# Kernel optimization log

Hardware: AMD Instinct MI355X
Metric: run time of the kernel (lower is better)

## Reference

```python
import jax, jax.numpy as jnp
import numpy as np
from jax import lax

THRESHOLD = 10.0  # p-norm threshold in HSEM
BN_EPS = 1e-5
DN = ('NCHW', 'OIHW', 'NCHW')


def setup_inputs() -> dict:
    key = jax.random.key(0)
    ks = jax.random.split(key, 9)
    b, c, h, w = 2, 256, 64, 64
    c_out = 512
    # scale x so pairwise L2 distances straddle the threshold (dense-ish hypergraph)
    x = jax.random.normal(ks[0], (b, c, h, w), dtype=jnp.float32) * 0.4
    fc_w = jax.random.normal(ks[1], (c, c), dtype=jnp.float32) * 0.02
    fc_b = jax.random.normal(ks[2], (c,), dtype=jnp.float32) * 0.02
    bn_gamma = jnp.ones((c,), dtype=jnp.float32)
    bn_beta = jnp.zeros((c,), dtype=jnp.float32)
    down_w = jax.random.normal(ks[3], (c, c, 3, 3), dtype=jnp.float32) * 0.02
    down_b = jax.random.normal(ks[4], (c,), dtype=jnp.float32) * 0.02
    out_w = jax.random.normal(ks[5], (c_out, c, 1, 1), dtype=jnp.float32) * 0.02
    out_b = jax.random.normal(ks[6], (c_out,), dtype=jnp.float32) * 0.02
    return {"x": x, "fc_w": fc_w, "fc_b": fc_b, "bn_gamma": bn_gamma,
            "bn_beta": bn_beta, "down_w": down_w, "down_b": down_b,
            "out_w": out_w, "out_b": out_b}


def _mean_agg(path, X):
    # path: [b, n_tgt, n_src], X: [b, n_src, d]; mean aggregation with inf->0 masking
    s = jnp.sum(path, axis=2, keepdims=True)           # [b, n_tgt, 1]
    norm = jnp.where(s > 0, 1.0 / jnp.where(s > 0, s, 1.0), 0.0)
    return norm * jnp.matmul(path, X)


def reference(x, fc_w, fc_b, bn_gamma, bn_beta, down_w, down_b, out_w, out_b):
    b, c, h, w = x.shape
    n = h * w
    xf = x.reshape(b, c, n).transpose(0, 2, 1)          # [b, n, c]
    # cdist (euclidean): ||a-b|| via expansion
    sq = jnp.sum(xf * xf, axis=-1)                      # [b, n]
    d2 = sq[:, :, None] + sq[:, None, :] - 2.0 * jnp.einsum('bnc,bmc->bnm', xf, xf)
    dist = jnp.sqrt(jnp.maximum(d2, 0.0))               # [b, n, n]
    hg = (dist < THRESHOLD).astype(x.dtype)             # dynamic hypergraph incidence
    # HyPConv: fc -> v2e (H^T) -> e2v (H)
    y = jnp.einsum('bnc,dc->bnd', xf, fc_w) + fc_b      # Linear(c1, c2)
    E = _mean_agg(jnp.swapaxes(hg, 1, 2), y)            # vertex -> edge
    v = _mean_agg(hg, E)                                # edge -> vertex
    xf = v + xf                                         # residual
    x4 = xf.transpose(0, 2, 1).reshape(b, c, h, w)
    # BatchNorm2d (training-mode batch statistics, biased var)
    mean = jnp.mean(x4, axis=(0, 2, 3))
    var = jnp.var(x4, axis=(0, 2, 3))
    xn = (x4 - mean[None, :, None, None]) * lax.rsqrt(var + BN_EPS)[None, :, None, None]
    xn = xn * bn_gamma[None, :, None, None] + bn_beta[None, :, None, None]
    xa = xn * jax.nn.sigmoid(xn)                        # SiLU
    # Downsample: pad (right=1, bottom=1) then 3x3 stride-2 VALID conv
    xp = jnp.pad(xa, ((0, 0), (0, 0), (0, 1), (0, 1)))
    xd = lax.conv_general_dilated(xp, down_w, (2, 2), 'VALID', dimension_numbers=DN)
    xd = xd + down_b[None, :, None, None]
    out = lax.conv_general_dilated(xd, out_w, (1, 1), 'VALID', dimension_numbers=DN)
    out = out + out_b[None, :, None, None]
    return out
```

## Files before the change

### kernel.cpp

```cpp
#include <hip/hip_runtime.h>
#include <hip/hip_bf16.h>
#include <math.h>

#define NPIX 4096
#define CH   256

#define OFF_XP    0u
#define OFF_XR    1048576u
#define OFF_VB    2097152u
#define OFF_TBS   3145728u
#define OFF_TBS2  4194304u
#define OFF_HG    5242880u
#define OFF_SQ    6291456u
#define OFF_PART  6299648u
#define OFF_BNSS  6365184u
#define OFF_DINV  6365696u
#define OFF_W3P   6373888u
#define OFF_WFCP  6668800u
#define OFF_WOUTP 6701568u

typedef __attribute__((ext_vector_type(8))) short bf16x8;
typedef __attribute__((ext_vector_type(16))) float f32x16;

static __device__ __forceinline__ short f2b(float f) {
  __hip_bfloat16 h = __float2bfloat16(f);
  return *reinterpret_cast<short*>(&h);
}
static __device__ __forceinline__ float b2f(short s) {
  union { unsigned u; float f; } r;
  r.u = ((unsigned)(unsigned short)s) << 16;
  return r.f;
}

static __device__ __forceinline__ bf16x8 byte2bf(unsigned byte) {
  union { unsigned u[4]; bf16x8 h; } r;
  r.u[0] = ((byte * 0x8001u) & 0x10001u) * 0x3F80u;
  r.u[1] = (((byte >> 2) * 0x8001u) & 0x10001u) * 0x3F80u;
  r.u[2] = (((byte >> 4) * 0x8001u) & 0x10001u) * 0x3F80u;
  r.u[3] = (((byte >> 6) * 0x8001u) & 0x10001u) * 0x3F80u;
  return r.h;
}

static __device__ __forceinline__ size_t packoff(int m, int c) {
  return ((size_t)((m >> 5) * 16 + (c >> 4)) * 2 + ((c >> 3) & 1)) * 256 + (m & 31) * 8 + (c & 7);
}

__global__ __launch_bounds__(256) void k_front2(const float* __restrict__ x,
                                                short* __restrict__ xp,
                                                float* __restrict__ sq,
                                                const float* __restrict__ fc_w,
                                                const float* __restrict__ ow,
                                                const float* __restrict__ dw,
                                                short* __restrict__ wfcp,
                                                short* __restrict__ woutp,
                                                short* __restrict__ w3p) {
  __shared__ float lds[256][33];
  __shared__ float red2[8][32];
  const int bid = blockIdx.x;
  const int t = threadIdx.x;
  if (bid < 256) {
    const int b = bid >> 7;
    const int n0 = (bid & 127) * 32;
    const float* xb = x + (size_t)b * CH * NPIX + n0;
    const int j = t & 31, cg8 = t >> 5;
#pragma unroll 4
    for (int it = 0; it < 32; ++it) {
      const int c = it * 8 + cg8;
      lds[c][j] = xb[(size_t)c * NPIX + j];
    }
    __syncthreads();
    {
      const int n = t & 31, cg = t >> 5;
      float s = 0.f;
#pragma unroll 8
      for (int i = 0; i < 32; ++i) {
        const float v = lds[cg * 32 + i][n];
        s += v * v;
      }
      red2[cg][n] = s;
    }
    short* xpb = xp + (size_t)b * NPIX * CH;
#pragma unroll
    for (int i = 0; i < 4; ++i) {
      const int f = i * 256 + t;
      const int n = f & 31, c0 = (f >> 5) * 8;
      short tmp[8];
#pragma unroll
      for (int k = 0; k < 8; ++k) tmp[k] = f2b(lds[c0 + k][n]);
      short* dst = xpb + packoff(n0 + n, c0);
      *(short4*)dst = *(short4*)&tmp[0];
      *(short4*)(dst + 4) = *(short4*)&tmp[4];
    }
    __syncthreads();
    if (t < 32) {
      float s = 0.f;
#pragma unroll
      for (int cg = 0; cg < 8; ++cg) s += red2[cg][t];
      sq[b * NPIX + n0 + t] = s;
    }
  } else {
    const int i = (bid - 256) * 256 + t;
    if (i < 65536) {
      wfcp[packoff(i >> 8, i & 255)] = f2b(fc_w[i]);
    } else if (i < 196608) {
      const int j = i - 65536;
      woutp[packoff(j >> 8, j & 255)] = f2b(ow[j]);
    } else {
      const int j = i - 196608;
      const int oc = j / 2304;
      const int rem = j % 2304;
      const int c = rem / 9, tap = rem % 9;
      const size_t off = ((size_t)((tap * 8 + (oc >> 5)) * 16 + (c >> 4)) * 2 + ((c >> 3) & 1)) * 256
                       + (oc & 31) * 8 + (c & 7);
      w3p[off] = f2b(dw[j]);
    }
  }
}

__global__ __launch_bounds__(128, 2) void k_gram4(const short* __restrict__ xp,
                                                  const float* __restrict__ sq,
                                                  unsigned* __restrict__ hgbit) {
  const int b = blockIdx.z;
  int tt = blockIdx.x;
  int bi = (int)((65.0f - sqrtf(4225.0f - 8.0f * (float)tt)) * 0.5f);
  bi = bi < 0 ? 0 : (bi > 31 ? 31 : bi);
  while (bi * (65 - bi) / 2 > tt) --bi;
  while ((bi + 1) * (64 - bi) / 2 <= tt) ++bi;
  const int bj = bi + (tt - bi * (65 - bi) / 2);
  const int i0 = bi * 128, j0 = bj * 128;

  const int t = threadIdx.x;
  const int lane = t & 63, w = t >> 6;
  const int c = lane & 31, h = lane >> 5;
  const short* xb = xp + (size_t)b * NPIX * CH;
  const int ibase = i0 + w * 64;
  const int jbase = j0;

  f32x16 acc[2][4];
#pragma unroll
  for (int m = 0; m < 2; ++m)
#pragma unroll
    for (int n = 0; n < 4; ++n)
#pragma unroll
      for (int r = 0; r < 16; ++r) acc[m][n][r] = 0.f;

  const short* pa = xb + (size_t)(ibase >> 5) * 8192 + lane * 8;
  const short* pb = xb + (size_t)(jbase >> 5) * 8192 + lane * 8;

#pragma unroll 2
  for (int kb = 0; kb < 16; ++kb) {
    const bf16x8 a0 = *(const bf16x8*)(pa + kb * 512);
    const bf16x8 a1 = *(const bf16x8*)(pa + 8192 + kb * 512);
    bf16x8 bb[4];
#pragma unroll
    for (int n = 0; n < 4; ++n) bb[n] = *(const bf16x8*)(pb + (size_t)n * 8192 + kb * 512);
#pragma unroll
    for (int n = 0; n < 4; ++n) {
      acc[0][n] = __builtin_amdgcn_mfma_f32_32x32x16_bf16(a0, bb[n], acc[0][n], 0, 0, 0);
      acc[1][n] = __builtin_amdgcn_mfma_f32_32x32x16_bf16(a1, bb[n], acc[1][n], 0, 0, 0);
    }
  }

  const int sqb = b * NPIX;
#pragma unroll
  for (int m = 0; m < 2; ++m) {
    float4 sqa[4];
#pragma unroll
    for (int q = 0; q < 4; ++q)
      sqa[q] = *(const float4*)(sq + sqb + ibase + m * 32 + q * 8 + 4 * h);
#pragma unroll
    for (int n = 0; n < 4; ++n) {
      const float sj = sq[sqb + jbase + n * 32 + c];
      const int wj = (jbase + n * 32) >> 5;
      unsigned mmask = 0u;
#pragma unroll
      for (int q = 0; q < 4; ++q) {
        const float sqq[4] = {sqa[q].x, sqa[q].y, sqa[q].z, sqa[q].w};
#pragma unroll
        for (int rr = 0; rr < 4; ++rr) {
          const int reg = q * 4 + rr;
          const float d2 = sqq[rr] + sj - 2.f * acc[m][n][reg];
          const bool cond = d2 < 100.f;
          const unsigned long long bal = __ballot(cond);
          if ((lane & 31) == reg) {
            const int row = ibase + m * 32 + rr + 8 * q + 4 * h;
            const unsigned wd = h ? (unsigned)(bal >> 32) : (unsigned)bal;
            hgbit[(size_t)(sqb + row) * 128 + wj] = wd;
          }
          mmask |= (cond ? 1u : 0u) << (rr + 8 * q + 4 * h);
        }
      }
      const unsigned merged = mmask | (unsigned)__shfl_xor((int)mmask, 32, 64);
      if (h == 0) {
        const int colg = jbase + n * 32 + c;
        hgbit[(size_t)(sqb + colg) * 128 + ((ibase + m * 32) >> 5)] = merged;
      }
    }
  }
}

__global__ __launch_bounds__(256) void k_fcdinv(const short* __restrict__ wfcp,
                                                const short* __restrict__ xp,
                                                short* __restrict__ C,
                                                const float* __restrict__ bias,
                                                const unsigned* __restrict__ hg,
                                                float* __restrict__ dinvf) {
  const int bid = blockIdx.x;
  const int t = threadIdx.x;
  if (bid >= 256) {
    const int row = (bid - 256) * 4 + (t >> 6);
    const int l = t & 63;
    const unsigned w0 = hg[(size_t)row * 128 + l * 2];
    const unsigned w1 = hg[(size_t)row * 128 + l * 2 + 1];
    int n = __popc(w0) + __popc(w1);
#pragma unroll
    for (int off = 32; off; off >>= 1) n += __shfl_down(n, off);
    if (l == 0) dinvf[row] = 1.0f / (float)n;
    return;
  }
  const int b = bid >> 7;
  const short* xpb = xp + (size_t)b * NPIX * CH;
  short* Cb = C + ((size_t)b << 20);
  const int l = t & 63, wid = t >> 6;
  const int m0 = ((bid >> 6) & 1) * 128 + wid * 32, n0 = (bid & 63) * 64;
  const int col = l & 31, half = l >> 5;
  f32x16 acc[2];
#pragma unroll
  for (int nt = 0; nt < 2; ++nt)
#pragma unroll
    for (int r = 0; r < 16; ++r) acc[nt][r] = 0.f;
  const short* pa = wfcp + (size_t)(m0 >> 5) * 8192 + l * 8;
  const short* pb = xpb + (size_t)(n0 >> 5) * 8192 + l * 8;
#pragma unroll 4
  for (int kb = 0; kb < 16; ++kb) {
    const bf16x8 a = *(const bf16x8*)(pa + kb * 512);
    const bf16x8 b0 = *(const bf16x8*)(pb + kb * 512);
    const bf16x8 b1 = *(const bf16x8*)(pb + 8192 + kb * 512);
    acc[0] = __builtin_amdgcn_mfma_f32_32x32x16_bf16(a, b0, acc[0], 0, 0, 0);
    acc[1] = __builtin_amdgcn_mfma_f32_32x32x16_bf16(a, b1, acc[1], 0, 0, 0);
  }
  const int cb = m0 >> 5;
#pragma unroll
  for (int nt = 0; nt < 2; ++nt) {
    const int node = n0 + nt * 32 + col;
    short* dst = Cb + ((size_t)cb * 512 + (node >> 3)) * 256 + (node & 7);
#pragma unroll
    for (int q = 0; q < 4; ++q)
#pragma unroll
      for (int rr = 0; rr < 4; ++rr) {
        const int c31 = rr + 8 * q + 4 * half;
        dst[c31 * 8] = f2b(acc[nt][q * 4 + rr] + bias[m0 + c31]);
      }
  }
}

__global__ __launch_bounds__(256) void k_hgemm_t4(const short* __restrict__ tbs,
                                                  const unsigned* __restrict__ hg,
                                                  const float* __restrict__ dinvf,
                                                  short* __restrict__ tbs2) {
  __shared__ float red[4][64][33];
  const int b = blockIdx.z;
  const int n0 = blockIdx.x * 64;
  const int cbp = blockIdx.y;
  const int ks = threadIdx.x >> 6;
  const int l = threadIdx.x & 63;
  const int col = l & 31, half = l >> 5;
  const int sh8 = half * 8;

  f32x16 acc00, acc01, acc10, acc11;
#pragma unroll
  for (int r = 0; r < 16; ++r) { acc00[r] = 0.f; acc01[r] = 0.f; acc10[r] = 0.f; acc11[r] = 0.f; }

  const short* pa0 = tbs + ((size_t)b << 20) + ((size_t)(cbp * 2) * 512 + half) * 256
                   + col * 8 + ks * 32768;
  const short* pa1 = pa0 + 131072;
  const uint4* hrow0 = (const uint4*)((const unsigned char*)hg
                     + ((size_t)b * NPIX + n0 + col) * 512 + ks * 128);
  const uint4* hrow1 = (const uint4*)((const unsigned char*)hg
                     + ((size_t)b * NPIX + n0 + 32 + col) * 512 + ks * 128);

#pragma unroll 2
  for (int o = 0; o < 8; ++o) {
    const uint4 wq0 = hrow0[o];
    const uint4 wq1 = hrow1[o];
    const unsigned ww0[4] = {wq0.x, wq0.y, wq0.z, wq0.w};
    const unsigned ww1[4] = {wq1.x, wq1.y, wq1.z, wq1.w};
#pragma unroll
    for (int s = 0; s < 4; ++s) {
      const bf16x8 a00 = *(const bf16x8*)(pa0);
      const bf16x8 a01 = *(const bf16x8*)(pa0 + 512);
      const bf16x8 a10 = *(const bf16x8*)(pa1);
      const bf16x8 a11 = *(const bf16x8*)(pa1 + 512);
      pa0 += 1024; pa1 += 1024;
      const bf16x8 b0 = byte2bf((ww0[s] >> sh8) & 0xFFu);
      const bf16x8 b1 = byte2bf((ww0[s] >> (16 + sh8)) & 0xFFu);
      const bf16x8 c0 = byte2bf((ww1[s] >> sh8) & 0xFFu);
      const bf16x8 c1 = byte2bf((ww1[s] >> (16 + sh8)) & 0xFFu);
      acc00 = __builtin_amdgcn_mfma_f32_32x32x16_bf16(a00, b0, acc00, 0, 0, 0);
      acc00 = __builtin_amdgcn_mfma_f32_32x32x16_bf16(a01, b1, acc00, 0, 0, 0);
      acc10 = __builtin_amdgcn_mfma_f32_32x32x16_bf16(a10, b0, acc10, 0, 0, 0);
      acc10 = __builtin_amdgcn_mfma_f32_32x32x16_bf16(a11, b1, acc10, 0, 0, 0);
      acc01 = __builtin_amdgcn_mfma_f32_32x32x16_bf16(a00, c0, acc01, 0, 0, 0);
      acc01 = __builtin_amdgcn_mfma_f32_32x32x16_bf16(a01, c1, acc01, 0, 0, 0);
      acc11 = __builtin_amdgcn_mfma_f32_32x32x16_bf16(a10, c0, acc11, 0, 0, 0);
      acc11 = __builtin_amdgcn_mfma_f32_32x32x16_bf16(a11, c1, acc11, 0, 0, 0);
    }
  }

#pragma unroll
  for (int r = 0; r < 16; ++r) { red[ks][l][r] = acc00[r]; red[ks][l][16 + r] = acc10[r]; }
  __syncthreads();
  {
    const int n = n0 + col;
    const float dinv = dinvf[b * NPIX + n];
    short* dst0 = tbs2 + ((size_t)b << 20) + ((size_t)(cbp * 2) * 512 + (n >> 3)) * 256 + (n & 7);
    short* dst1 = dst0 + 131072;
#pragma unroll
    for (int rj = 0; rj < 8; ++rj) {
      const int reg = ks * 8 + rj;
      const float s = red[0][l][reg] + red[1][l][reg] + red[2][l][reg] + red[3][l][reg];
      const int rm = reg & 15;
      const int c31 = (rm & 3) + 8 * (rm >> 2) + 4 * half;
      (reg < 16 ? dst0 : dst1)[c31 * 8] = f2b(s * dinv);
    }
  }
  __syncthreads();
#pragma unroll
  for (int r = 0; r < 16; ++r) { red[ks][l][r] = acc01[r]; red[ks][l][16 + r] = acc11[r]; }
  __syncthreads();
  {
    const int n = n0 + 32 + col;
    const float dinv = dinvf[b * NPIX + n];
    short* dst0 = tbs2 + ((size_t)b << 20) + ((size_t)(cbp * 2) * 512 + (n >> 3)) * 256 + (n & 7);
    short* dst1 = dst0 + 131072;
#pragma unroll
    for (int rj = 0; rj < 8; ++rj) {
      const int reg = ks * 8 + rj;
      const float s = red[0][l][reg] + red[1][l][reg] + red[2][l][reg] + red[3][l][reg];
      const int rm = reg & 15;
      const int c31 = (rm & 3) + 8 * (rm >> 2) + 4 * half;
      (reg < 16 ? dst0 : dst1)[c31 * 8] = f2b(s * dinv);
    }
  }
}

__global__ __launch_bounds__(256) void k_hgemm_n4(const unsigned* __restrict__ hg,
                                                  const short* __restrict__ tbs2,
                                                  const float* __restrict__ dinvf,
                                                  const short* __restrict__ xp,
                                                  short* __restrict__ vb,
                                                  float* __restrict__ part) {
  __shared__ float red[4][64][33];
  __shared__ float bnp[128];
  const int b = blockIdx.z;
  const int cbp = blockIdx.x;
  const int m0 = blockIdx.y * 64;
  const int ks = threadIdx.x >> 6;
  const int l = threadIdx.x & 63;
  const int col = l & 31, half = l >> 5;
  const int sh8 = half * 8;
  if (threadIdx.x < 128) bnp[threadIdx.x] = 0.f;

  f32x16 acc00, acc01, acc10, acc11;
#pragma unroll
  for (int r = 0; r < 16; ++r) { acc00[r] = 0.f; acc01[r] = 0.f; acc10[r] = 0.f; acc11[r] = 0.f; }

  const short* pb0 = tbs2 + ((size_t)b << 20) + ((size_t)(cbp * 2) * 512 + half) * 256
                   + col * 8 + ks * 32768;
  const short* pb1 = pb0 + 131072;
  const uint4* hrow0 = (const uint4*)((const unsigned char*)hg
                     + ((size_t)b * NPIX + m0 + col) * 512 + ks * 128);
  const uint4* hrow1 = (const uint4*)((const unsigned char*)hg
                     + ((size_t)b * NPIX + m0 + 32 + col) * 512 + ks * 128);

#pragma unroll 2
  for (int o = 0; o < 8; ++o) {
    const uint4 wq0 = hrow0[o];
    const uint4 wq1 = hrow1[o];
    const unsigned ww0[4] = {wq0.x, wq0.y, wq0.z, wq0.w};
    const unsigned ww1[4] = {wq1.x, wq1.y, wq1.z, wq1.w};
#pragma unroll
    for (int s = 0; s < 4; ++s) {
      const bf16x8 b00 = *(const bf16x8*)(pb0);
      const bf16x8 b01 = *(const bf16x8*)(pb0 + 512);
      const bf16x8 b10 = *(const bf16x8*)(pb1);
      const bf16x8 b11 = *(const bf16x8*)(pb1 + 512);
      pb0 += 1024; pb1 += 1024;
      const bf16x8 a0 = byte2bf((ww0[s] >> sh8) & 0xFFu);
      const bf16x8 a1 = byte2bf((ww0[s] >> (16 + sh8)) & 0xFFu);
      const bf16x8 a2 = byte2bf((ww1[s] >> sh8) & 0xFFu);
      const bf16x8 a3 = byte2bf((ww1[s] >> (16 + sh8)) & 0xFFu);
      acc00 = __builtin_amdgcn_mfma_f32_32x32x16_bf16(a0, b00, acc00, 0, 0, 0);
      acc00 = __builtin_amdgcn_mfma_f32_32x32x16_bf16(a1, b01, acc00, 0, 0, 0);
      acc01 = __builtin_amdgcn_mfma_f32_32x32x16_bf16(a0, b10, acc01, 0, 0, 0);
      acc01 = __builtin_amdgcn_mfma_f32_32x32x16_bf16(a1, b11, acc01, 0, 0, 0);
      acc10 = __builtin_amdgcn_mfma_f32_32x32x16_bf16(a2, b00, acc10, 0, 0, 0);
      acc10 = __builtin_amdgcn_mfma_f32_32x32x16_bf16(a3, b01, acc10, 0, 0, 0);
      acc11 = __builtin_amdgcn_mfma_f32_32x32x16_bf16(a2, b10, acc11, 0, 0, 0);
      acc11 = __builtin_amdgcn_mfma_f32_32x32x16_bf16(a3, b11, acc11, 0, 0, 0);
    }
  }

  const short* xpb = xp + (size_t)b * NPIX * CH;
#pragma unroll
  for (int r = 0; r < 16; ++r) { red[ks][l][r] = acc00[r]; red[ks][l][16 + r] = acc01[r]; }
  __syncthreads();
  {
    const int cc = cbp * 64 + col;
#pragma unroll
    for (int rj = 0; rj < 8; ++rj) {
      const int reg = ks * 8 + rj;
      const float s = red[0][l][reg] + red[1][l][reg] + red[2][l][reg] + red[3][l][reg];
      const int rm = reg & 15;
      const int r = m0 + (rm & 3) + 8 * (rm >> 2) + 4 * half;
      const int ccc = cc + (reg < 16 ? 0 : 32);
      const size_t o = ((size_t)(b * NPIX + r)) * CH + ccc;
      const short sv = f2b(s * dinvf[b * NPIX + r] + b2f(xpb[packoff(r, ccc)]));
      vb[o] = sv;
      const float vr = b2f(sv);
      const int ci = col + (reg < 16 ? 0 : 32);
      atomicAdd(&bnp[ci], vr);
      atomicAdd(&bnp[64 + ci], vr * vr);
    }
  }
  __syncthreads();
#pragma unroll
  for (int r = 0; r < 16; ++r) { red[ks][l][r] = acc10[r]; red[ks][l][16 + r] = acc11[r]; }
  __syncthreads();
  {
    const int cc = cbp * 64 + col;
#pragma unroll
    for (int rj = 0; rj < 8; ++rj) {
      const int reg = ks * 8 + rj;
      const float s = red[0][l][reg] + red[1][l][reg] + red[2][l][reg] + red[3][l][reg];
      const int rm = reg & 15;
      const int r = m0 + 32 + (rm & 3) + 8 * (rm >> 2) + 4 * half;
      const int ccc = cc + (reg < 16 ? 0 : 32);
      const size_t o = ((size_t)(b * NPIX + r)) * CH + ccc;
      const short sv = f2b(s * dinvf[b * NPIX + r] + b2f(xpb[packoff(r, ccc)]));
      vb[o] = sv;
      const float vr = b2f(sv);
      const int ci = col + (reg < 16 ? 0 : 32);
      atomicAdd(&bnp[ci], vr);
      atomicAdd(&bnp[64 + ci], vr * vr);
    }
  }
  __syncthreads();
  if (threadIdx.x < 128) {
    const int slot = b * 64 + blockIdx.y;
    part[((size_t)(cbp * 128 + slot)) * 128 + threadIdx.x] = bnp[threadIdx.x];
  }
}

__global__ void k_bnfin(const float* __restrict__ part, const float* __restrict__ gamma,
                        const float* __restrict__ beta, float* __restrict__ bnss) {
  const int t = threadIdx.x;
  const int cbp = t >> 6, ch = t & 63;
  float s = 0.f, ss = 0.f;
  for (int i = 0; i < 128; ++i) {
    const float* p = part + ((size_t)(cbp * 128 + i)) * 128;
    s += p[ch];
    ss += p[64 + ch];
  }
  const float mean = s * (1.f / 8192.f);
  const float var = ss * (1.f / 8192.f) - mean * mean;
  const float inv = rsqrtf(var + 1e-5f);
  const float sc = gamma[t] * inv;
  bnss[t] = sc;
  bnss[256 + t] = beta[t] - mean * sc;
}

__global__ void k_bnapply3(const short* __restrict__ vb, const float* __restrict__ bnss,
                           short* __restrict__ xpp) {
  const int i = blockIdx.x * 256 + threadIdx.x;
  const short4 sv = reinterpret_cast<const short4*>(vb)[i];
  const int c0 = (i & 63) * 4;
  const int n = (i >> 6) & 4095;
  const int b = i >> 18;
  const float4 sc = *(const float4*)(bnss + c0);
  const float4 sh = *(const float4*)(bnss + 256 + c0);
  const float u0 = b2f(sv.x) * sc.x + sh.x;
  const float u1 = b2f(sv.y) * sc.y + sh.y;
  const float u2 = b2f(sv.z) * sc.z + sh.z;
  const float u3 = b2f(sv.w) * sc.w + sh.w;
  short4 o;
  o.x = f2b(u0 / (1.f + expf(-u0)));
  o.y = f2b(u1 / (1.f + expf(-u1)));
  o.z = f2b(u2 / (1.f + expf(-u2)));
  o.w = f2b(u3 / (1.f + expf(-u3)));
  const int ih = n >> 6, iw = n & 63;
  const int p = iw & 1, ow = iw >> 1;
  const size_t off = ((size_t)(((b * 2 + p) * 64 + ih) * 16 + (c0 >> 4)) * 2 + ((c0 >> 3) & 1)) * 256
                   + ow * 8 + (c0 & 7);
  *(short4*)(xpp + off) = o;
}

__global__ __launch_bounds__(64) void k_conv5(const short* __restrict__ xpp,
                                              const short* __restrict__ w3p,
                                              float* __restrict__ convp) {
  const int ocg = blockIdx.x;
  const int oh = blockIdx.y;
  const int bz = blockIdx.z;
  const int b = bz & 1, cs = bz >> 1;
  const int l = threadIdx.x;
  const int col = l & 31;
  const bf16x8 zv = {0, 0, 0, 0, 0, 0, 0, 0};

  f32x16 acc;
#pragma unroll
  for (int r = 0; r < 16; ++r) acc[r] = 0.f;

  for (int kh = 0; kh < 3; ++kh) {
    const int ih = 2 * oh + kh;
    if (ih >= 64) continue;
#pragma unroll
    for (int kw = 0; kw < 3; ++kw) {
      const int p = kw & 1;
      const short* pa = xpp + ((size_t)((b * 2 + p) * 64 + ih) * 16 + cs * 4) * 512
                      + l * 8 + (kw == 2 ? 8 : 0);
      const short* pb = w3p + ((size_t)((kh * 3 + kw) * 8 + ocg) * 16 + cs * 4) * 512 + l * 8;
      const bool kill = (kw == 2) && (col == 31);
#pragma unroll
      for (int kb = 0; kb < 4; ++kb) {
        bf16x8 a = *(const bf16x8*)(pa + kb * 512);
        if (kill) a = zv;
        const bf16x8 bb = *(const bf16x8*)(pb + kb * 512);
        acc = __builtin_amdgcn_mfma_f32_32x32x16_bf16(a, bb, acc, 0, 0, 0);
      }
    }
  }
  const int half = l >> 5;
  const int oc = ocg * 32 + col;
#pragma unroll
  for (int q = 0; q < 4; ++q)
#pragma unroll
    for (int rr = 0; rr < 4; ++rr) {
      const int ow = rr + 8 * q + 4 * half;
      convp[((size_t)bz * 1024 + oh * 32 + ow) * 256 + oc] = acc[q * 4 + rr];
    }
}

__global__ void k_convmerge3(const float* __restrict__ convp, const float* __restrict__ db,
                             short* __restrict__ xdtb) {
  const int i = blockIdx.x * 256 + threadIdx.x;
  const int b = i >> 16, px = (i >> 6) & 1023, oc0 = (i & 63) * 4;
  const size_t base = ((size_t)px) * 256 + oc0;
  const float4 h0 = *(const float4*)(convp + ((size_t)(0 + b) << 18) + base);
  const float4 h1 = *(const float4*)(convp + ((size_t)(2 + b) << 18) + base);
  const float4 h2 = *(const float4*)(convp + ((size_t)(4 + b) << 18) + base);
  const float4 h3 = *(const float4*)(convp + ((size_t)(6 + b) << 18) + base);
  const float4 bv = *(const float4*)(db + oc0);
  short4 o;
  o.x = f2b(h0.x + h1.x + h2.x + h3.x + bv.x);
  o.y = f2b(h0.y + h1.y + h2.y + h3.y + bv.y);
  o.z = f2b(h0.z + h1.z + h2.z + h3.z + bv.z);
  o.w = f2b(h0.w + h1.w + h2.w + h3.w + bv.w);
  const size_t off = ((size_t)((b * 32 + (px >> 5)) * 16 + (oc0 >> 4)) * 2 + ((oc0 >> 3) & 1)) * 256
                   + (px & 31) * 8 + (oc0 & 7);
  *(short4*)(xdtb + off) = o;
}

__global__ __launch_bounds__(256) void k_mfma_nt2(const short* __restrict__ woutp,
                                                  const short* __restrict__ xdtb,
                                                  float* __restrict__ C,
                                                  const float* __restrict__ bias) {
  const int b = blockIdx.z;
  xdtb += (size_t)b * 1024 * CH;
  C += (size_t)b * 512 * 1024;
  const int t = threadIdx.x, l = t & 63, wid = t >> 6;
  const int m0 = blockIdx.y * 128 + wid * 32, n0 = blockIdx.x * 64;
  const int col = l & 31, half = l >> 5;
  f32x16 acc[2];
#pragma unroll
  for (int nt = 0; nt < 2; ++nt)
#pragma unroll
    for (int r = 0; r < 16; ++r) acc[nt][r] = 0.f;
  const short* pa = woutp + (size_t)(m0 >> 5) * 8192 + l * 8;
  const short* pb = xdtb + (size_t)(n0 >> 5) * 8192 + l * 8;
#pragma unroll 4
  for (int kb = 0; kb < 16; ++kb) {
    const bf16x8 a = *(const bf16x8*)(pa + kb * 512);
    const bf16x8 b0 = *(const bf16x8*)(pb + kb * 512);
    const bf16x8 b1 = *(const bf16x8*)(pb + 8192 + kb * 512);
    acc[0] = __builtin_amdgcn_mfma_f32_32x32x16_bf16(a, b0, acc[0], 0, 0, 0);
    acc[1] = __builtin_amdgcn_mfma_f32_32x32x16_bf16(a, b1, acc[1], 0, 0, 0);
  }
#pragma unroll
  for (int nt = 0; nt < 2; ++nt) {
#pragma unroll
    for (int q = 0; q < 4; ++q)
#pragma unroll
      for (int rr = 0; rr < 4; ++rr) {
        const int row = m0 + rr + 8 * q + 4 * half;
        const int cc = n0 + nt * 32 + col;
        C[(size_t)row * 1024 + cc] = acc[nt][q * 4 + rr] + bias[row];
      }
  }
}

extern "C" void kernel_launch(void* const* d_in, const int* in_sizes, int n_in,
                              void* d_out, int out_size, void* d_ws, size_t ws_size,
                              hipStream_t stream) {
  const float* x     = (const float*)d_in[0];
  const float* fc_w  = (const float*)d_in[1];
  const float* fc_b  = (const float*)d_in[2];
  const float* gamma = (const float*)d_in[3];
  const float* beta  = (const float*)d_in[4];
  const float* dw    = (const float*)d_in[5];
  const float* db    = (const float*)d_in[6];
  const float* ow    = (const float*)d_in[7];
  const float* ob    = (const float*)d_in[8];

  float* ws   = (float*)d_ws;
  short* xp   = (short*)(ws + OFF_XP);
  float* convp= ws + OFF_XP;
  short* vb   = (short*)(ws + OFF_VB);
  short* tbs  = (short*)(ws + OFF_TBS);
  short* xdtb = (short*)(ws + OFF_TBS);
  short* tbs2 = (short*)(ws + OFF_TBS2);
  short* xpp  = (short*)(ws + OFF_TBS2);
  unsigned* hg = (unsigned*)(ws + OFF_HG);
  float* sqv  = ws + OFF_SQ;
  float* part = ws + OFF_PART;
  float* bnss = ws + OFF_BNSS;
  float* dinvf= ws + OFF_DINV;
  short* w3p  = (short*)(ws + OFF_W3P);
  short* wfcp = (short*)(ws + OFF_WFCP);
  short* woutp= (short*)(ws + OFF_WOUTP);
  float* out  = (float*)d_out;

  k_front2<<<3328, 256, 0, stream>>>(x, xp, sqv, fc_w, ow, dw, wfcp, woutp, w3p);
  k_gram4<<<dim3(528, 1, 2), 128, 0, stream>>>(xp, sqv, hg);
  k_fcdinv<<<2304, 256, 0, stream>>>(wfcp, xp, tbs, fc_b, hg, dinvf);
  k_hgemm_t4<<<dim3(64, 4, 2), 256, 0, stream>>>(tbs, hg, dinvf, tbs2);
  k_hgemm_n4<<<dim3(4, 64, 2), 256, 0, stream>>>(hg, tbs2, dinvf, xp, vb, part);
  k_bnfin<<<1, 256, 0, stream>>>(part, gamma, beta, bnss);
  k_bnapply3<<<2048, 256, 0, stream>>>(vb, bnss, xpp);
  k_conv5<<<dim3(8, 32, 8), 64, 0, stream>>>(xpp, w3p, convp);
  k_convmerge3<<<512, 256, 0, stream>>>(convp, db, xdtb);
  k_mfma_nt2<<<dim3(16, 4, 2), 256, 0, stream>>>(woutp, xdtb, out, ob);
}
```

Baseline: 140.4 us.

## Double split-K waves in hypergraph GEMMs and move BN statistics to separate kernel

Both hypergraph aggregation GEMMs now use 512 threads per block, splitting the K dimension across 8 waves instead of 4, with a larger shared-memory reduction buffer. The aim is more waves per block to hide the latency of the global loads. The per-element shared atomics that accumulated BatchNorm sums in the second GEMM are removed, and a new k_bnstat kernel recomputes per-channel sums from vb instead. This adds a kernel launch and a re-read of vb, and the larger shared buffer may lower occupancy.

```diff
diff --git a/kernel.cpp b/kernel.cpp
--- a/kernel.cpp
+++ b/kernel.cpp
@@ -254,11 +254,11 @@
   }
 }
 
-__global__ __launch_bounds__(256) void k_hgemm_t4(const short* __restrict__ tbs,
+__global__ __launch_bounds__(512) void k_hgemm_t5(const short* __restrict__ tbs,
                                                   const unsigned* __restrict__ hg,
                                                   const float* __restrict__ dinvf,
                                                   short* __restrict__ tbs2) {
-  __shared__ float red[4][64][33];
+  __shared__ float red[8][64][33];
   const int b = blockIdx.z;
   const int n0 = blockIdx.x * 64;
   const int cbp = blockIdx.y;
@@ -272,15 +272,15 @@
   for (int r = 0; r < 16; ++r) { acc00[r] = 0.f; acc01[r] = 0.f; acc10[r] = 0.f; acc11[r] = 0.f; }
 
   const short* pa0 = tbs + ((size_t)b << 20) + ((size_t)(cbp * 2) * 512 + half) * 256
-                   + col * 8 + ks * 32768;
+                   + col * 8 + ks * 16384;
   const short* pa1 = pa0 + 131072;
   const uint4* hrow0 = (const uint4*)((const unsigned char*)hg
-                     + ((size_t)b * NPIX + n0 + col) * 512 + ks * 128);
+                     + ((size_t)b * NPIX + n0 + col) * 512 + ks * 64);
   const uint4* hrow1 = (const uint4*)((const unsigned char*)hg
-                     + ((size_t)b * NPIX + n0 + 32 + col) * 512 + ks * 128);
-
-#pragma unroll 2
-  for (int o = 0; o < 8; ++o) {
+                     + ((size_t)b * NPIX + n0 + 32 + col) * 512 + ks * 64);
+
+#pragma unroll
+  for (int o = 0; o < 4; ++o) {
     const uint4 wq0 = hrow0[o];
     const uint4 wq1 = hrow1[o];
     const unsigned ww0[4] = {wq0.x, wq0.y, wq0.z, wq0.w};
@@ -316,9 +316,11 @@
     short* dst0 = tbs2 + ((size_t)b << 20) + ((size_t)(cbp * 2) * 512 + (n >> 3)) * 256 + (n & 7);
     short* dst1 = dst0 + 131072;
 #pragma unroll
-    for (int rj = 0; rj < 8; ++rj) {
-      const int reg = ks * 8 + rj;
-      const float s = red[0][l][reg] + red[1][l][reg] + red[2][l][reg] + red[3][l][reg];
+    for (int rj = 0; rj < 4; ++rj) {
+      const int reg = ks * 4 + rj;
+      float s = 0.f;
+#pragma unroll
+      for (int w = 0; w < 8; ++w) s += red[w][l][reg];
       const int rm = reg & 15;
       const int c31 = (rm & 3) + 8 * (rm >> 2) + 4 * half;
       (reg < 16 ? dst0 : dst1)[c31 * 8] = f2b(s * dinv);
@@ -334,9 +336,11 @@
     short* dst0 = tbs2 + ((size_t)b << 20) + ((size_t)(cbp * 2) * 512 + (n >> 3)) * 256 + (n & 7);
     short* dst1 = dst0 + 131072;
 #pragma unroll
-    for (int rj = 0; rj < 8; ++rj) {
-      const int reg = ks * 8 + rj;
-      const float s = red[0][l][reg] + red[1][l][reg] + red[2][l][reg] + red[3][l][reg];
+    for (int rj = 0; rj < 4; ++rj) {
+      const int reg = ks * 4 + rj;
+      float s = 0.f;
+#pragma unroll
+      for (int w = 0; w < 8; ++w) s += red[w][l][reg];
       const int rm = reg & 15;
       const int c31 = (rm & 3) + 8 * (rm >> 2) + 4 * half;
       (reg < 16 ? dst0 : dst1)[c31 * 8] = f2b(s * dinv);
@@ -344,14 +348,12 @@
   }
 }
 
-__global__ __launch_bounds__(256) void k_hgemm_n4(const unsigned* __restrict__ hg,
+__global__ __launch_bounds__(512) void k_hgemm_n5(const unsigned* __restrict__ hg,
                                                   const short* __restrict__ tbs2,
                                                   const float* __restrict__ dinvf,
                                                   const short* __restrict__ xp,
-                                                  short* __restrict__ vb,
-                                                  float* __restrict__ part) {
-  __shared__ float red[4][64][33];
-  __shared__ float bnp[128];
+                                                  short* __restrict__ vb) {
+  __shared__ float red[8][64][33];
   const int b = blockIdx.z;
   const int cbp = blockIdx.x;
   const int m0 = blockIdx.y * 64;
@@ -359,22 +361,21 @@
   const int l = threadIdx.x & 63;
   const int col = l & 31, half = l >> 5;
   const int sh8 = half * 8;
-  if (threadIdx.x < 128) bnp[threadIdx.x] = 0.f;
 
   f32x16 acc00, acc01, acc10, acc11;
 #pragma unroll
   for (int r = 0; r < 16; ++r) { acc00[r] = 0.f; acc01[r] = 0.f; acc10[r] = 0.f; acc11[r] = 0.f; }
 
   const short* pb0 = tbs2 + ((size_t)b << 20) + ((size_t)(cbp * 2) * 512 + half) * 256
-                   + col * 8 + ks * 32768;
+                   + col * 8 + ks * 16384;
   const short* pb1 = pb0 + 131072;
   const uint4* hrow0 = (const uint4*)((const unsigned char*)hg
-                     + ((size_t)b * NPIX + m0 + col) * 512 + ks * 128);
+                     + ((size_t)b * NPIX + m0 + col) * 512 + ks * 64);
   const uint4* hrow1 = (const uint4*)((const unsigned char*)hg
-                     + ((size_t)b * NPIX + m0 + 32 + col) * 512 + ks * 128);
-
-#pragma unroll 2
-  for (int o = 0; o < 8; ++o) {
+                     + ((size_t)b * NPIX + m0 + 32 + col) * 512 + ks * 64);
+
+#pragma unroll
+  for (int o = 0; o < 4; ++o) {
     const uint4 wq0 = hrow0[o];
     const uint4 wq1 = hrow1[o];
     const unsigned ww0[4] = {wq0.x, wq0.y, wq0.z, wq0.w};
@@ -408,19 +409,16 @@
   {
     const int cc = cbp * 64 + col;
 #pragma unroll
-    for (int rj = 0; rj < 8; ++rj) {
-      const int reg = ks * 8 + rj;
-      const float s = red[0][l][reg] + red[1][l][reg] + red[2][l][reg] + red[3][l][reg];
+    for (int rj = 0; rj < 4; ++rj) {
+      const int reg = ks * 4 + rj;
+      float s = 0.f;
+#pragma unroll
+      for (int w = 0; w < 8; ++w) s += red[w][l][reg];
       const int rm = reg & 15;
       const int r = m0 + (rm & 3) + 8 * (rm >> 2) + 4 * half;
       const int ccc = cc + (reg < 16 ? 0 : 32);
       const size_t o = ((size_t)(b * NPIX + r)) * CH + ccc;
-      const short sv = f2b(s * dinvf[b * NPIX + r] + b2f(xpb[packoff(r, ccc)]));
-      vb[o] = sv;
-      const float vr = b2f(sv);
-      const int ci = col + (reg < 16 ? 0 : 32);
-      atomicAdd(&bnp[ci], vr);
-      atomicAdd(&bnp[64 + ci], vr * vr);
+      vb[o] = f2b(s * dinvf[b * NPIX + r] + b2f(xpb[packoff(r, ccc)]));
     }
   }
   __syncthreads();
@@ -430,38 +428,37 @@
   {
     const int cc = cbp * 64 + col;
 #pragma unroll
-    for (int rj = 0; rj < 8; ++rj) {
-      const int reg = ks * 8 + rj;
-      const float s = red[0][l][reg] + red[1][l][reg] + red[2][l][reg] + red[3][l][reg];
+    for (int rj = 0; rj < 4; ++rj) {
+      const int reg = ks * 4 + rj;
+      float s = 0.f;
+#pragma unroll
+      for (int w = 0; w < 8; ++w) s += red[w][l][reg];
       const int rm = reg & 15;
       const int r = m0 + 32 + (rm & 3) + 8 * (rm >> 2) + 4 * half;
       const int ccc = cc + (reg < 16 ? 0 : 32);
       const size_t o = ((size_t)(b * NPIX + r)) * CH + ccc;
-      const short sv = f2b(s * dinvf[b * NPIX + r] + b2f(xpb[packoff(r, ccc)]));
-      vb[o] = sv;
-      const float vr = b2f(sv);
-      const int ci = col + (reg < 16 ? 0 : 32);
-      atomicAdd(&bnp[ci], vr);
-      atomicAdd(&bnp[64 + ci], vr * vr);
-    }
-  }
-  __syncthreads();
-  if (threadIdx.x < 128) {
-    const int slot = b * 64 + blockIdx.y;
-    part[((size_t)(cbp * 128 + slot)) * 128 + threadIdx.x] = bnp[threadIdx.x];
-  }
+      vb[o] = f2b(s * dinvf[b * NPIX + r] + b2f(xpb[packoff(r, ccc)]));
+    }
+  }
+}
+
+__global__ void k_bnstat(const short* __restrict__ vb, float* __restrict__ part) {
+  const int t = threadIdx.x, blk = blockIdx.x;
+  float s = 0.f, ss = 0.f;
+  const short* p = vb + (size_t)blk * 64 * CH;
+  for (int r = 0; r < 64; ++r) {
+    const float v = b2f(p[r * CH + t]);
+    s += v; ss += v * v;
+  }
+  part[blk * 512 + t] = s;
+  part[blk * 512 + 256 + t] = ss;
 }
 
 __global__ void k_bnfin(const float* __restrict__ part, const float* __restrict__ gamma,
                         const float* __restrict__ beta, float* __restrict__ bnss) {
   const int t = threadIdx.x;
-  const int cbp = t >> 6, ch = t & 63;
   float s = 0.f, ss = 0.f;
-  for (int i = 0; i < 128; ++i) {
-    const float* p = part + ((size_t)(cbp * 128 + i)) * 128;
-    s += p[ch];
-    ss += p[64 + ch];
-  }
+  for (int i = 0; i < 128; ++i) { s += part[i * 512 + t]; ss += part[i * 512 + 256 + t]; }
   const float mean = s * (1.f / 8192.f);
   const float var = ss * (1.f / 8192.f) - mean * mean;
   const float inv = rsqrtf(var + 1e-5f);
@@ -632,8 +629,9 @@
   k_front2<<<3328, 256, 0, stream>>>(x, xp, sqv, fc_w, ow, dw, wfcp, woutp, w3p);
   k_gram4<<<dim3(528, 1, 2), 128, 0, stream>>>(xp, sqv, hg);
   k_fcdinv<<<2304, 256, 0, stream>>>(wfcp, xp, tbs, fc_b, hg, dinvf);
-  k_hgemm_t4<<<dim3(64, 4, 2), 256, 0, stream>>>(tbs, hg, dinvf, tbs2);
-  k_hgemm_n4<<<dim3(4, 64, 2), 256, 0, stream>>>(hg, tbs2, dinvf, xp, vb, part);
+  k_hgemm_t5<<<dim3(64, 4, 2), 512, 0, stream>>>(tbs, hg, dinvf, tbs2);
+  k_hgemm_n5<<<dim3(4, 64, 2), 512, 0, stream>>>(hg, tbs2, dinvf, xp, vb);
+  k_bnstat<<<128, 256, 0, stream>>>(vb, part);
   k_bnfin<<<1, 256, 0, stream>>>(part, gamma, beta, bnss);
   k_bnapply3<<<2048, 256, 0, stream>>>(vb, bnss, xpp);
   k_conv5<<<dim3(8, 32, 8), 64, 0, stream>>>(xpp, w3p, convp);
```

New measurement: 132.6 us. -5.6%, faster.
